# Performance work log

Hardware: AMD Instinct MI355X
Metric: run time of the kernel (lower is better)

Reference implementation:

```python
import math
import jax, jax.numpy as jnp
from jax import lax
import numpy as np

C = 19
SIZE = 33
MIOU = [0.95, 0.78, 0.88, 0.45, 0.48, 0.55, 0.6, 0.7, 0.9, 0.58, 0.92,
        0.75, 0.5, 0.91, 0.62, 0.7, 0.55, 0.42, 0.68]


def _class_weights(mious):
    mious = np.asarray(mious, dtype=np.float64)
    ratios = 1.0 / (mious / (mious.sum() + 1e-6) + 1e-6)
    r_max, r_min = ratios.max(), ratios.min()
    w = (ratios - r_min + 1e-6) / (r_max - r_min + 1e-6)
    return jnp.asarray(w, dtype=jnp.float32)


def setup_inputs() -> dict:
    key = jax.random.key(0)
    logit = jax.random.normal(key, (1, C, 1024, 2048), dtype=jnp.float32)
    return {"logit": logit, "class_weights": _class_weights(MIOU)}


def reference(logit, class_weights):
    x = logit[0]                                   # [C, H, W]
    p = jax.nn.softmax(x, axis=0)                  # [C, H, W]
    predict = jnp.argmax(p, axis=0)                # [H, W] int
    one_hot = jax.nn.one_hot(predict, C, dtype=jnp.float32)   # [H, W, C]
    one_hot = jnp.transpose(one_hot, (2, 0, 1))[None]          # [1, C, H, W]

    # 33x33 box filter, depthwise (groups=C), zero padding 16 (SAME)
    k_dw = jnp.ones((C, 1, SIZE, SIZE), dtype=jnp.float32)
    summary = lax.conv_general_dilated(one_hot, k_dw, (1, 1), 'SAME',
                                       feature_group_count=C)   # [1,C,H,W]
    count = jnp.sum(summary, axis=1, keepdims=True)              # [1,1,H,W]
    dist = summary / count
    region_impurity = jnp.sum(-dist * jnp.log(dist + 1e-6), axis=1,
                              keepdims=True) / math.log(19)      # [1,1,H,W]

    pixel_entropy = jnp.sum(-p * jnp.log(p + 1e-6), axis=0)       # [H, W]
    # per-pixel class-indexed weight gather (replaces the CPU loop)
    wt_pixel_entropy = pixel_entropy * class_weights[predict]     # [H, W]
    wt_pixel_entropy = wt_pixel_entropy[None, None] / math.log(19)

    k1 = jnp.ones((1, 1, SIZE, SIZE), dtype=jnp.float32)
    region_sum_entropy = lax.conv_general_dilated(wt_pixel_entropy, k1,
                                                  (1, 1), 'SAME')
    prediction_uncertainty = region_sum_entropy / count
    score = region_impurity * prediction_uncertainty
    return (score[0, 0], region_impurity[0, 0], prediction_uncertainty[0, 0])
```

## Files before the change

kernel.cpp:

```cpp
#include <hip/hip_runtime.h>
#include <stdint.h>

#define HH 1024
#define WW 2048
#define HWC (HH * WW)
#define NC 19
#define WP 2080
#define RAD 16
static constexpr float INV_LN19 = 1.0f / 2.9444389791664403f;

static __device__ __forceinline__ int imin(int a, int b) { return a < b ? a : b; }
static __device__ __forceinline__ int imax(int a, int b) { return a > b ? a : b; }

__global__ __launch_bounds__(256) void k1_pix(const float* __restrict__ logit,
                                              const float* __restrict__ cw,
                                              uint8_t* __restrict__ predict,
                                              float* __restrict__ wtent) {
    int t = blockIdx.x * 256 + threadIdx.x;
    int p0 = t * 4;
    float xx[4][NC];
#pragma unroll
    for (int c = 0; c < NC; ++c) {
        float4 v = *reinterpret_cast<const float4*>(logit + (size_t)c * HWC + p0);
        xx[0][c] = v.x; xx[1][c] = v.y; xx[2][c] = v.z; xx[3][c] = v.w;
    }
    float went[4];
    int ids[4];
#pragma unroll
    for (int e = 0; e < 4; ++e) {
        float m = xx[e][0]; int id = 0;
#pragma unroll
        for (int c = 1; c < NC; ++c) { if (xx[e][c] > m) { m = xx[e][c]; id = c; } }
        float s = 0.f, u = 0.f;
#pragma unroll
        for (int c = 0; c < NC; ++c) {
            float d = xx[e][c] - m;
            float ex = __expf(d);
            s += ex;
            u = fmaf(ex, d, u);
        }
        float ent = __logf(s) - u / s;
        went[e] = ent * cw[id] * INV_LN19;
        ids[e] = id;
    }
    uint32_t packed = (uint32_t)ids[0] | ((uint32_t)ids[1] << 8) |
                      ((uint32_t)ids[2] << 16) | ((uint32_t)ids[3] << 24);
    *reinterpret_cast<uint32_t*>(predict + p0) = packed;
    *reinterpret_cast<float4*>(wtent + p0) = make_float4(went[0], went[1], went[2], went[3]);
}

__global__ void k2_pad(uint8_t* __restrict__ hist, float* __restrict__ colent) {
    int t = blockIdx.x * 256 + threadIdx.x;
    const uint4 z = make_uint4(0u, 0u, 0u, 0u);
    if (t < NC * HH) {
        uint8_t* row = hist + (size_t)t * WP;
        *reinterpret_cast<uint4*>(row) = z;
        *reinterpret_cast<uint4*>(row + 2064) = z;
    } else {
        int r = t - NC * HH;
        float* row = colent + (size_t)r * WP;
#pragma unroll
        for (int k = 0; k < 4; ++k) {
            *reinterpret_cast<uint4*>(row + 4 * k) = z;
            *reinterpret_cast<uint4*>(row + 2064 + 4 * k) = z;
        }
    }
}

#define SEG 16
__global__ __launch_bounds__(256) void k2_vert(const uint8_t* __restrict__ predict,
                                               const float* __restrict__ wtent,
                                               uint8_t* __restrict__ hist,
                                               float* __restrict__ colent) {
    int w = blockIdx.x * 64 + (threadIdx.x & 63);
    int seg = blockIdx.y * 4 + (threadIdx.x >> 6);
    int r0 = seg * SEG;
    int cnt[NC];
#pragma unroll
    for (int c = 0; c < NC; ++c) cnt[c] = 0;
    float es = 0.f;
    for (int h = r0 - RAD; h < r0 + RAD; ++h) {
        if (h >= 0) {
            int pin = predict[(size_t)h * WW + w];
#pragma unroll
            for (int c = 0; c < NC; ++c) cnt[c] += (pin == c);
            es += wtent[(size_t)h * WW + w];
        }
    }
    for (int r = r0; r < r0 + SEG; ++r) {
        int ha = r + RAD;
        if (ha < HH) {
            int pin = predict[(size_t)ha * WW + w];
#pragma unroll
            for (int c = 0; c < NC; ++c) cnt[c] += (pin == c);
            es += wtent[(size_t)ha * WW + w];
        }
        size_t rowoff = (size_t)r * WP + RAD + w;
#pragma unroll
        for (int c = 0; c < NC; ++c)
            hist[(size_t)c * HH * WP + rowoff] = (uint8_t)cnt[c];
        colent[rowoff] = es;
        int hs = r - RAD;
        if (hs >= 0) {
            int pin = predict[(size_t)hs * WW + w];
#pragma unroll
            for (int c = 0; c < NC; ++c) cnt[c] -= (pin == c);
            es -= wtent[(size_t)hs * WW + w];
        }
    }
}

#define TR 32
#define TC 128
__global__ __launch_bounds__(256) void k3_horiz(const uint8_t* __restrict__ hist,
                                                const float* __restrict__ colent,
                                                float* __restrict__ out) {
    __shared__ float smem[TR * 165];
    uint32_t* smem_u = reinterpret_cast<uint32_t*>(smem);

    int r0 = blockIdx.y * TR;
    int w0 = blockIdx.x * TC;
    int row = threadIdx.x >> 3;
    int seg = threadIdx.x & 7;
    int r = r0 + row;
    int c0 = seg * 16;
    float nh = (float)(imin(r + RAD, HH - 1) - imax(r - RAD, 0) + 1);
    float rcpN[16], imp[16];
#pragma unroll
    for (int j = 0; j < 16; ++j) {
        int wc = w0 + c0 + j;
        float nw = (float)(imin(wc + RAD, WW - 1) - imax(wc - RAD, 0) + 1);
        rcpN[j] = 1.0f / (nh * nw);
        imp[j] = 0.f;
    }
    for (int c = 0; c < NC; ++c) {
        __syncthreads();
        const uint32_t* src = reinterpret_cast<const uint32_t*>(hist + (size_t)c * HH * WP);
#pragma unroll
        for (int i = 0; i < 5; ++i) {
            int k = threadIdx.x + i * 256;
            int rr = k / 40, cc = k % 40;
            smem_u[rr * 41 + cc] = src[(size_t)(r0 + rr) * (WP / 4) + (w0 >> 2) + cc];
        }
        __syncthreads();
        const uint32_t* sp = smem_u + row * 41 + (c0 >> 2);
        uint32_t d[12];
#pragma unroll
        for (int k = 0; k < 12; ++k) d[k] = sp[k];
        int run = 0;
#pragma unroll
        for (int k = 0; k < 8; ++k)
            run += (int)(d[k] & 255) + (int)((d[k] >> 8) & 255) +
                   (int)((d[k] >> 16) & 255) + (int)(d[k] >> 24);
#pragma unroll
        for (int j = 0; j < 16; ++j) {
            int ein  = (int)((d[8 + (j >> 2)] >> (8 * (j & 3))) & 255);
            int eout = (int)((d[j >> 2]       >> (8 * (j & 3))) & 255);
            int n = run + ein;
            float dist = (float)n * rcpN[j];
            imp[j] = fmaf(dist, __logf(dist + 1e-6f), imp[j]);
            run = n - eout;
        }
    }
    __syncthreads();
#pragma unroll
    for (int i = 0; i < 20; ++i) {
        int k = threadIdx.x + i * 256;
        int rr = k / 160, cc = k % 160;
        smem[rr * 165 + cc] = colent[(size_t)(r0 + rr) * WP + w0 + cc];
    }
    __syncthreads();
    const float* ep = smem + row * 165 + c0;
    float erun = 0.f;
#pragma unroll
    for (int k = 0; k < 32; ++k) erun += ep[k];
#pragma unroll
    for (int j = 0; j < 16; ++j) {
        float esum = erun + ep[j + 32];
        float unc = esum * rcpN[j];
        float rim = imp[j] * (-INV_LN19);
        int wc = w0 + c0 + j;
        size_t o = (size_t)r * WW + wc;
        out[o] = rim * unc;
        out[HWC + o] = rim;
        out[2 * HWC + o] = unc;
        erun = esum - ep[j];
    }
}

extern "C" void kernel_launch(void* const* d_in, const int* in_sizes, int n_in,
                              void* d_out, int out_size, void* d_ws, size_t ws_size,
                              hipStream_t stream) {
    const float* logit = (const float*)d_in[0];
    const float* cw = (const float*)d_in[1];
    float* out = (float*)d_out;
    uint8_t* ws = (uint8_t*)d_ws;

    uint8_t* predict = ws;
    float* wtent = (float*)(ws + 2097152);
    float* colent = (float*)(ws + 10485760);
    uint8_t* hist = ws + 19005440;

    k1_pix<<<2048, 256, 0, stream>>>(logit, cw, predict, wtent);
    k2_pad<<<80, 256, 0, stream>>>(hist, colent);
    k2_vert<<<dim3(32, 16), 256, 0, stream>>>(predict, wtent, hist, colent);
    k3_horiz<<<dim3(16, 32), 256, 0, stream>>>(hist, colent, out);
}
```

Baseline: 335.6 us.

## Fuse vertical box-sum and horizontal pass into one shared-memory tiled kernel

Replaces the separate padding, vertical sliding-window and horizontal kernels with one kernel. Each block loads a haloed tile of predictions and weighted entropy into shared memory and computes the vertical window sums there, per class. This removes the large per-class byte histogram and the column-entropy intermediates that made a round trip through global memory. In exchange it recomputes halo rows in every tile, runs the per-class vertical counting with only 160 active threads, and uses about 51KB of shared memory per block, which limits occupancy.

Result: faster. 315.8 us (-5.9%).

```diff
diff --git a/kernel.cpp b/kernel.cpp
--- a/kernel.cpp
+++ b/kernel.cpp
@@ -5,7 +5,6 @@
 #define WW 2048
 #define HWC (HH * WW)
 #define NC 19
-#define WP 2080
 #define RAD 16
 static constexpr float INV_LN19 = 1.0f / 2.9444389791664403f;
 
@@ -49,81 +48,64 @@
     *reinterpret_cast<float4*>(wtent + p0) = make_float4(went[0], went[1], went[2], went[3]);
 }
 
-__global__ void k2_pad(uint8_t* __restrict__ hist, float* __restrict__ colent) {
-    int t = blockIdx.x * 256 + threadIdx.x;
-    const uint4 z = make_uint4(0u, 0u, 0u, 0u);
-    if (t < NC * HH) {
-        uint8_t* row = hist + (size_t)t * WP;
-        *reinterpret_cast<uint4*>(row) = z;
-        *reinterpret_cast<uint4*>(row + 2064) = z;
-    } else {
-        int r = t - NC * HH;
-        float* row = colent + (size_t)r * WP;
+#define TR 32
+#define TC 128
+#define IR 64
+#define IC 160
+__global__ __launch_bounds__(256) void k23_fused(const uint8_t* __restrict__ predict,
+                                                 const float* __restrict__ wtent,
+                                                 float* __restrict__ out) {
+    __shared__ __align__(16) char smem[51712];
+    uint8_t*  sp8  = reinterpret_cast<uint8_t*>(smem);
+    uint32_t* sp32 = reinterpret_cast<uint32_t*>(smem);
+    float*    swt  = reinterpret_cast<float*>(smem + 10240);
+    float*    sce  = swt;
+    uint32_t* scnt = reinterpret_cast<uint32_t*>(smem + 30720);
+
+    int tid = threadIdx.x;
+    int r0 = blockIdx.y * TR;
+    int w0 = blockIdx.x * TC;
+
 #pragma unroll
-        for (int k = 0; k < 4; ++k) {
-            *reinterpret_cast<uint4*>(row + 4 * k) = z;
-            *reinterpret_cast<uint4*>(row + 2064 + 4 * k) = z;
+    for (int i = 0; i < 10; ++i) {
+        int k = tid + i * 256;
+        int rr = k / 40, cc = k - rr * 40;
+        int grow = r0 - RAD + rr;
+        int gcb = w0 - RAD + cc * 4;
+        uint32_t v = 0xFFFFFFFFu;
+        if ((unsigned)grow < HH && (unsigned)gcb < WW)
+            v = *reinterpret_cast<const uint32_t*>(predict + (size_t)grow * WW + gcb);
+        sp32[rr * 40 + cc] = v;
+    }
+#pragma unroll
+    for (int i = 0; i < 40; ++i) {
+        int k = tid + i * 256;
+        int rr = k / 160, cc = k - rr * 160;
+        int grow = r0 - RAD + rr;
+        int gc = w0 - RAD + cc;
+        float v = 0.f;
+        if ((unsigned)grow < HH && (unsigned)gc < WW)
+            v = wtent[(size_t)grow * WW + gc];
+        swt[rr * 160 + cc] = v;
+    }
+    __syncthreads();
+
+    if (tid < IC) {
+        float es = 0.f;
+#pragma unroll
+        for (int h = 0; h < 32; ++h) es += swt[h * 160 + tid];
+        for (int rr = 0; rr < 32; ++rr) {
+            float tmp = swt[rr * 160 + tid];
+            es += swt[(rr + 32) * 160 + tid];
+            sce[rr * 160 + tid] = es;
+            es -= tmp;
         }
     }
-}
 
-#define SEG 16
-__global__ __launch_bounds__(256) void k2_vert(const uint8_t* __restrict__ predict,
-                                               const float* __restrict__ wtent,
-                                               uint8_t* __restrict__ hist,
-                                               float* __restrict__ colent) {
-    int w = blockIdx.x * 64 + (threadIdx.x & 63);
-    int seg = blockIdx.y * 4 + (threadIdx.x >> 6);
-    int r0 = seg * SEG;
-    int cnt[NC];
-#pragma unroll
-    for (int c = 0; c < NC; ++c) cnt[c] = 0;
-    float es = 0.f;
-    for (int h = r0 - RAD; h < r0 + RAD; ++h) {
-        if (h >= 0) {
-            int pin = predict[(size_t)h * WW + w];
-#pragma unroll
-            for (int c = 0; c < NC; ++c) cnt[c] += (pin == c);
-            es += wtent[(size_t)h * WW + w];
-        }
-    }
-    for (int r = r0; r < r0 + SEG; ++r) {
-        int ha = r + RAD;
-        if (ha < HH) {
-            int pin = predict[(size_t)ha * WW + w];
-#pragma unroll
-            for (int c = 0; c < NC; ++c) cnt[c] += (pin == c);
-            es += wtent[(size_t)ha * WW + w];
-        }
-        size_t rowoff = (size_t)r * WP + RAD + w;
-#pragma unroll
-        for (int c = 0; c < NC; ++c)
-            hist[(size_t)c * HH * WP + rowoff] = (uint8_t)cnt[c];
-        colent[rowoff] = es;
-        int hs = r - RAD;
-        if (hs >= 0) {
-            int pin = predict[(size_t)hs * WW + w];
-#pragma unroll
-            for (int c = 0; c < NC; ++c) cnt[c] -= (pin == c);
-            es -= wtent[(size_t)hs * WW + w];
-        }
-    }
-}
-
-#define TR 32
-#define TC 128
-__global__ __launch_bounds__(256) void k3_horiz(const uint8_t* __restrict__ hist,
-                                                const float* __restrict__ colent,
-                                                float* __restrict__ out) {
-    __shared__ float smem[TR * 165];
-    uint32_t* smem_u = reinterpret_cast<uint32_t*>(smem);
-
-    int r0 = blockIdx.y * TR;
-    int w0 = blockIdx.x * TC;
-    int row = threadIdx.x >> 3;
-    int seg = threadIdx.x & 7;
+    int row = tid >> 3;
+    int seg = tid & 7;
+    int c0 = seg * 16;
     int r = r0 + row;
-    int c0 = seg * 16;
     float nh = (float)(imin(r + RAD, HH - 1) - imax(r - RAD, 0) + 1);
     float rcpN[16], imp[16];
 #pragma unroll
@@ -133,44 +115,34 @@
         rcpN[j] = 1.0f / (nh * nw);
         imp[j] = 0.f;
     }
+
     for (int c = 0; c < NC; ++c) {
         __syncthreads();
-        const uint32_t* src = reinterpret_cast<const uint32_t*>(hist + (size_t)c * HH * WP);
+        if (tid < IC) {
+            int cnt = 0;
 #pragma unroll
-        for (int i = 0; i < 5; ++i) {
-            int k = threadIdx.x + i * 256;
-            int rr = k / 40, cc = k % 40;
-            smem_u[rr * 41 + cc] = src[(size_t)(r0 + rr) * (WP / 4) + (w0 >> 2) + cc];
+            for (int h = 0; h < 32; ++h) cnt += (sp8[h * 160 + tid] == c);
+            for (int rr = 0; rr < 32; ++rr) {
+                cnt += (sp8[(rr + 32) * 160 + tid] == c);
+                scnt[rr * 164 + tid] = (uint32_t)cnt;
+                cnt -= (sp8[rr * 160 + tid] == c);
+            }
         }
         __syncthreads();
-        const uint32_t* sp = smem_u + row * 41 + (c0 >> 2);
-        uint32_t d[12];
-#pragma unroll
-        for (int k = 0; k < 12; ++k) d[k] = sp[k];
+        const uint32_t* base = scnt + row * 164 + c0;
         int run = 0;
 #pragma unroll
-        for (int k = 0; k < 8; ++k)
-            run += (int)(d[k] & 255) + (int)((d[k] >> 8) & 255) +
-                   (int)((d[k] >> 16) & 255) + (int)(d[k] >> 24);
+        for (int k = 0; k < 32; ++k) run += (int)base[k];
 #pragma unroll
         for (int j = 0; j < 16; ++j) {
-            int ein  = (int)((d[8 + (j >> 2)] >> (8 * (j & 3))) & 255);
-            int eout = (int)((d[j >> 2]       >> (8 * (j & 3))) & 255);
-            int n = run + ein;
+            int n = run + (int)base[j + 32];
             float dist = (float)n * rcpN[j];
             imp[j] = fmaf(dist, __logf(dist + 1e-6f), imp[j]);
-            run = n - eout;
+            run = n - (int)base[j];
         }
     }
-    __syncthreads();
-#pragma unroll
-    for (int i = 0; i < 20; ++i) {
-        int k = threadIdx.x + i * 256;
-        int rr = k / 160, cc = k % 160;
-        smem[rr * 165 + cc] = colent[(size_t)(r0 + rr) * WP + w0 + cc];
-    }
-    __syncthreads();
-    const float* ep = smem + row * 165 + c0;
+
+    const float* ep = sce + row * 160 + c0;
     float erun = 0.f;
 #pragma unroll
     for (int k = 0; k < 32; ++k) erun += ep[k];
@@ -198,11 +170,7 @@
 
     uint8_t* predict = ws;
     float* wtent = (float*)(ws + 2097152);
-    float* colent = (float*)(ws + 10485760);
-    uint8_t* hist = ws + 19005440;
 
     k1_pix<<<2048, 256, 0, stream>>>(logit, cw, predict, wtent);
-    k2_pad<<<80, 256, 0, stream>>>(hist, colent);
-    k2_vert<<<dim3(32, 16), 256, 0, stream>>>(predict, wtent, hist, colent);
-    k3_horiz<<<dim3(16, 32), 256, 0, stream>>>(hist, colent, out);
+    k23_fused<<<dim3(WW / TC, HH / TR), 256, 0, stream>>>(predict, wtent, out);
 }
```
